# Kernel optimization log

Measured on AMD Instinct MI355X. Metric: run time of the kernel, lower is better.

Reference implementation:

```python
import jax, jax.numpy as jnp
import numpy as np

T, B, C = 1024, 16, 1024
H, K, PAD = 16, 7, 6  # num_heads, kernel_size, padding_l (causal)
R = C // H


def setup_inputs() -> dict:
    key = jax.random.key(0)
    kx, kw = jax.random.split(key)
    x = jax.random.normal(kx, (T, B, C), dtype=jnp.float32)
    # xavier_uniform for weight_linear.weight of shape (H*K, C)
    bound = float(np.sqrt(6.0 / (C + H * K)))
    W = jax.random.uniform(kw, (H * K, C), dtype=jnp.float32, minval=-bound, maxval=bound)
    return {"x": x, "W": W}


def reference(x, W):
    Tn, Bn, Cn = x.shape
    # dynamic per-position conv weights: (T, B, H, K)
    w = jnp.einsum('tbc,oc->tbo', x, W).reshape(Tn, Bn, H, K)

    # band structure: row t attends absolute positions t + k - PAD, k in [0, K)
    pos = jnp.arange(Tn)[:, None] + jnp.arange(K)[None, :] - PAD     # (T, K)
    valid = (pos >= 0) & (pos < Tn)                                   # (T, K)
    logits = jnp.where(valid[:, None, None, :], w, -jnp.inf)
    wsm = jax.nn.softmax(logits, axis=-1)                             # (T, B, H, K), zeros off-band

    # windowed weighted sum (the bmm against the band matrix, done directly)
    pc = jnp.clip(pos, 0, Tn - 1)                                     # (T, K)
    xh = x.reshape(Tn, Bn, H, R)
    xg = xh[pc]                                                       # (T, K, B, H, R)
    out = jnp.einsum('tbhk,tkbhr->tbhr', wsm, xg).reshape(Tn, Bn, Cn)

    # dense (B*H, T, T) softmaxed band matrix, as returned by the torch module
    w_bht = wsm.transpose(1, 2, 0, 3).reshape(Bn * H, Tn, K)
    dense = jnp.zeros((Bn * H, Tn, Tn), wsm.dtype)
    dense = dense.at[:, jnp.arange(Tn)[:, None], pc].add(jnp.where(valid, w_bht, 0.0))
    return out, dense
```

## Files before the change

kernel.cpp:

```cpp
#include <hip/hip_runtime.h>
#include <math.h>

#define TT 1024
#define BB 16
#define CC 1024
#define HH 16
#define KK 7
#define PADL 6
#define HK 112
#define LSTRIDE 116

typedef short bf16x8 __attribute__((ext_vector_type(8)));
typedef float f32x4 __attribute__((ext_vector_type(4)));

__device__ __forceinline__ short f2bf(float f) {
    union { float f; unsigned u; } v; v.f = f;
    unsigned r = v.u + 0x7fff + ((v.u >> 16) & 1);
    return (short)(r >> 16);
}

__global__ __launch_bounds__(256) void k0_cvtW(const float* __restrict__ W,
                                               short* __restrict__ Wb) {
    const int i = (blockIdx.x * 256 + threadIdx.x) * 8;
    const float4 a0 = *(const float4*)(W + i);
    const float4 a1 = *(const float4*)(W + i + 4);
    bf16x8 v;
    v[0] = f2bf(a0.x); v[1] = f2bf(a0.y); v[2] = f2bf(a0.z); v[3] = f2bf(a0.w);
    v[4] = f2bf(a1.x); v[5] = f2bf(a1.y); v[6] = f2bf(a1.z); v[7] = f2bf(a1.w);
    *(bf16x8*)(Wb + i) = v;
}

__global__ __launch_bounds__(256) void k1_mfma(const float* __restrict__ x,
                                               const short* __restrict__ Wb,
                                               float* __restrict__ wsm) {
    __shared__ __align__(16) float Llog[4][16 * LSTRIDE];
    __shared__ __align__(16) float Lout[4][16 * HK];

    const int tid = threadIdx.x;
    const int w = tid >> 6;
    const int lane = tid & 63;
    const int quad = lane >> 4;
    const int lr = lane & 15;
    const int strip = blockIdx.x * 4 + w;
    const int r0 = strip * 16;

    bf16x8 ap, bp;
#pragma unroll
    for (int e = 0; e < 8; ++e) {
        const int k = quad * 8 + e;
        ap[e] = (k == lr) ? (short)0x3F80 : (short)0;
        bp[e] = f2bf((float)k);
    }
    f32x4 pz = (f32x4){0.f, 0.f, 0.f, 0.f};
    pz = __builtin_amdgcn_mfma_f32_16x16x32_bf16(ap, bp, pz, 0, 0, 0);
    const bool claim = (pz[0] == (float)(quad * 4)) &&
                       (pz[1] == (float)(quad * 4 + 1));

    const float* __restrict__ xa = x + (size_t)(r0 + lr) * CC + quad * 8;
    const short* __restrict__ wb = Wb + (size_t)lr * CC + quad * 8;

    f32x4 acc[7];
#pragma unroll
    for (int j = 0; j < 7; ++j) acc[j] = (f32x4){0.f, 0.f, 0.f, 0.f};

#pragma unroll 4
    for (int k0 = 0; k0 < CC; k0 += 32) {
        const float4 a0 = *(const float4*)(xa + k0);
        const float4 a1 = *(const float4*)(xa + k0 + 4);
        bf16x8 af;
        af[0] = f2bf(a0.x); af[1] = f2bf(a0.y); af[2] = f2bf(a0.z); af[3] = f2bf(a0.w);
        af[4] = f2bf(a1.x); af[5] = f2bf(a1.y); af[6] = f2bf(a1.z); af[7] = f2bf(a1.w);
#pragma unroll
        for (int j = 0; j < 7; ++j) {
            const bf16x8 bfrag = *(const bf16x8*)(wb + (size_t)(j * 16) * CC + k0);
            acc[j] = __builtin_amdgcn_mfma_f32_16x16x32_bf16(af, bfrag, acc[j], 0, 0, 0);
        }
    }

#pragma unroll
    for (int j = 0; j < 7; ++j)
#pragma unroll
        for (int r = 0; r < 4; ++r) {
            const int rowi = claim ? (quad * 4 + r) : lr;
            const int coli = claim ? lr : (quad * 4 + r);
            Llog[w][rowi * LSTRIDE + j * 16 + coli] = acc[j][r];
        }
    __syncthreads();

    const int kmin = (strip >= PADL) ? 0 : (PADL - strip);
#pragma unroll
    for (int p = 0; p < 4; ++p) {
        const int idx = p * 64 + lane;
        const int m = idx >> 4;
        const int h = idx & 15;
        const float* lp = &Llog[w][m * LSTRIDE + h * KK];
        float a[KK];
#pragma unroll
        for (int k = 0; k < KK; ++k) a[k] = lp[k];

        float mx = -INFINITY;
#pragma unroll
        for (int k = 0; k < KK; ++k)
            if (k >= kmin) mx = fmaxf(mx, a[k]);
        float e[KK], s = 0.f;
#pragma unroll
        for (int k = 0; k < KK; ++k) {
            if (k >= kmin) { e[k] = expf(a[k] - mx); s += e[k]; }
            else           { e[k] = 0.f; }
        }
        const float inv = 1.f / s;
        float* op = &Lout[w][m * HK + h * KK];
#pragma unroll
        for (int k = 0; k < KK; ++k) op[k] = e[k] * inv;
    }
    __syncthreads();

    float* __restrict__ dst = wsm + (size_t)r0 * HK;
    const float* __restrict__ src = &Lout[w][0];
#pragma unroll
    for (int i = 0; i < 7; ++i) {
        const int o = i * 256 + lane * 4;
        *(float4*)(dst + o) = *(const float4*)(src + o);
    }
}

__global__ __launch_bounds__(256) void k23_fused(const float* __restrict__ x,
                                                 const float* __restrict__ wsm,
                                                 float* __restrict__ dense,
                                                 float* __restrict__ out) {
    __shared__ float Lband[16][8];
    const int blk = blockIdx.x;

    if ((blk % 5) == 0) {
        const int r0 = (blk / 5) << 2;
        const int t = r0 >> 4;
        const int c = threadIdx.x << 2;
        const int h = c >> 6;
        const int kmin = (t >= PADL) ? 0 : (PADL - t);

#pragma unroll
        for (int i = 0; i < 4; ++i) {
            const int row = r0 + i;
            const float* __restrict__ wp = wsm + ((size_t)row * HH + h) * KK;
            float w[KK];
#pragma unroll
            for (int k = 0; k < KK; ++k) w[k] = wp[k];

            f32x4 acc = (f32x4){0.f, 0.f, 0.f, 0.f};
            for (int k = kmin; k < KK; ++k) {
                const f32x4 xv = *(const f32x4*)(
                    x + ((size_t)row + (size_t)(k - PADL) * BB) * CC + c);
                acc[0] += w[k] * xv[0];
                acc[1] += w[k] * xv[1];
                acc[2] += w[k] * xv[2];
                acc[3] += w[k] * xv[3];
            }
            __builtin_nontemporal_store(acc,
                (f32x4*)(out + (size_t)row * CC + c));
        }
    } else {
        const int blk2 = blk - (blk / 5) - 1;
        const int bh = blk2 >> 6;
        const int tc = blk2 & 63;
        const int b = bh >> 4;
        const int h = bh & 15;
        const int t0 = tc * 16;
        const int tid = threadIdx.x;

        if (tid < 112) {
            const int r = tid & 15;
            const int j = tid >> 4;
            Lband[r][j] =
                wsm[(((size_t)(t0 + r) * BB + b) * HH + h) * KK + j];
        }
        __syncthreads();

        const int col = tid << 2;
        float* __restrict__ drow =
            dense + ((size_t)bh * TT + t0) * TT + col;

#pragma unroll
        for (int i = 0; i < 16; ++i) {
            const int t = t0 + i;
            const int lo = t - PADL;
            f32x4 v = (f32x4){0.f, 0.f, 0.f, 0.f};
            if (col + 3 >= lo && col <= t) {
#pragma unroll
                for (int j = 0; j < 4; ++j) {
                    const int cc = col + j;
                    if (cc >= lo && cc <= t && cc >= 0)
                        v[j] = Lband[i][cc - lo];
                }
            }
            *(f32x4*)drow = v;
            drow += TT;
        }
    }
}

extern "C" void kernel_launch(void* const* d_in, const int* in_sizes, int n_in,
                              void* d_out, int out_size, void* d_ws, size_t ws_size,
                              hipStream_t stream) {
    const float* x = (const float*)d_in[0];
    const float* W = (const float*)d_in[1];
    float* out = (float*)d_out;
    float* dense = out + (size_t)TT * BB * CC;
    float* wsm = (float*)d_ws;
    short* Wb = (short*)(wsm + (size_t)TT * BB * HK);

    k0_cvtW<<<56, 256, 0, stream>>>(W, Wb);
    k1_mfma<<<256, 256, 0, stream>>>(x, Wb, wsm);
    k23_fused<<<5 * (TT * BB) / 4, 256, 0, stream>>>(x, wsm, dense, out);
}
```

Baseline: 1.205 ms.

## Zero dense matrix in GEMM kernel, write only band windows afterward

```diff
diff --git a/kernel.cpp b/kernel.cpp
--- a/kernel.cpp
+++ b/kernel.cpp
@@ -30,18 +30,31 @@
     *(bf16x8*)(Wb + i) = v;
 }
 
-__global__ __launch_bounds__(256) void k1_mfma(const float* __restrict__ x,
-                                               const short* __restrict__ Wb,
-                                               float* __restrict__ wsm) {
+__global__ __launch_bounds__(256) void kA(const float* __restrict__ x,
+                                          const short* __restrict__ Wb,
+                                          float* __restrict__ wsm,
+                                          float* __restrict__ dense) {
     __shared__ __align__(16) float Llog[4][16 * LSTRIDE];
     __shared__ __align__(16) float Lout[4][16 * HK];
 
+    const int blk = blockIdx.x;
     const int tid = threadIdx.x;
+
+    if (blk >= 256) {
+        const size_t NF4 = (size_t)BB * HH * TT * TT / 4;
+        const size_t stride = (size_t)1792 * 256;
+        f32x4* __restrict__ p = (f32x4*)dense;
+        const f32x4 z = (f32x4){0.f, 0.f, 0.f, 0.f};
+        for (size_t i = (size_t)(blk - 256) * 256 + tid; i < NF4; i += stride)
+            p[i] = z;
+        return;
+    }
+
     const int w = tid >> 6;
     const int lane = tid & 63;
     const int quad = lane >> 4;
     const int lr = lane & 15;
-    const int strip = blockIdx.x * 4 + w;
+    const int strip = blk * 4 + w;
     const int r0 = strip * 16;
 
     bf16x8 ap, bp;
@@ -124,10 +137,10 @@
     }
 }
 
-__global__ __launch_bounds__(256) void k23_fused(const float* __restrict__ x,
-                                                 const float* __restrict__ wsm,
-                                                 float* __restrict__ dense,
-                                                 float* __restrict__ out) {
+__global__ __launch_bounds__(256) void kB(const float* __restrict__ x,
+                                          const float* __restrict__ wsm,
+                                          float* __restrict__ dense,
+                                          float* __restrict__ out) {
     __shared__ float Lband[16][8];
     const int blk = blockIdx.x;
 
@@ -175,25 +188,22 @@
         }
         __syncthreads();
 
-        const int col = tid << 2;
-        float* __restrict__ drow =
-            dense + ((size_t)bh * TT + t0) * TT + col;
-
-#pragma unroll
-        for (int i = 0; i < 16; ++i) {
-            const int t = t0 + i;
-            const int lo = t - PADL;
-            f32x4 v = (f32x4){0.f, 0.f, 0.f, 0.f};
-            if (col + 3 >= lo && col <= t) {
-#pragma unroll
-                for (int j = 0; j < 4; ++j) {
-                    const int cc = col + j;
-                    if (cc >= lo && cc <= t && cc >= 0)
-                        v[j] = Lband[i][cc - lo];
-                }
+        const int r = tid >> 4;
+        const int thrj = tid & 15;
+        const int t = t0 + r;
+        const int lo = t - PADL;
+        const int S = (t >= PADL) ? ((t - PADL) >> 5) : 0;
+        const int col0 = S * 32 + thrj * 4;
+
+        if (col0 < TT) {
+            f32x4 v;
+#pragma unroll
+            for (int l = 0; l < 4; ++l) {
+                const int col = col0 + l;
+                v[l] = (col >= lo && col <= t && col >= 0)
+                           ? Lband[r][col - lo] : 0.f;
             }
-            *(f32x4*)drow = v;
-            drow += TT;
+            *(f32x4*)(dense + ((size_t)bh * TT + t) * TT + col0) = v;
         }
     }
 }
@@ -209,6 +219,6 @@
     short* Wb = (short*)(wsm + (size_t)TT * BB * HK);
 
     k0_cvtW<<<56, 256, 0, stream>>>(W, Wb);
-    k1_mfma<<<256, 256, 0, stream>>>(x, Wb, wsm);
-    k23_fused<<<5 * (TT * BB) / 4, 256, 0, stream>>>(x, wsm, dense, out);
-}
+    kA<<<2048, 256, 0, stream>>>(x, Wb, wsm, dense);
+    kB<<<5 * (TT * BB) / 4, 256, 0, stream>>>(x, wsm, dense, out);
+}
```

New measurement: 1.216 ms. No clear change (+0.9%).
